# Kernel tuning notes

Hardware: AMD Instinct MI355X
Metric: run time of the kernel (lower is better)

Reference implementation:

```python
import jax, jax.numpy as jnp
import numpy as np

N = 100000
E = 1600000
F_IN = 128
F_OUT = 128
EPS = 1e-5


def setup_inputs() -> dict:
    key = jax.random.key(0)
    ks = jax.random.split(key, 6)
    x = jax.random.normal(ks[0], (N, F_IN), dtype=jnp.float32)
    edge_index = jax.random.randint(ks[1], (2, E), 0, N, dtype=jnp.int32)
    edge_weight = jax.random.uniform(ks[2], (E,), dtype=jnp.float32)
    gamma = jnp.ones((F_IN,), dtype=jnp.float32)
    beta = jnp.zeros((F_IN,), dtype=jnp.float32)
    W = jax.random.normal(ks[3], (F_OUT, F_IN), dtype=jnp.float32) * (1.0 / np.sqrt(F_IN))
    b = jnp.zeros((F_OUT,), dtype=jnp.float32)
    return {"x": x, "edge_index": edge_index, "edge_weight": edge_weight,
            "gamma": gamma, "beta": beta, "W": W, "b": b}


def reference(x, edge_index, edge_weight, gamma, beta, W, b):
    # LayerNorm (elementwise affine) + ReLU; dropout_mask=None (eval path)
    mean = jnp.mean(x, axis=-1, keepdims=True)
    var = jnp.mean(jnp.square(x - mean), axis=-1, keepdims=True)
    xn = (x - mean) * jax.lax.rsqrt(var + EPS) * gamma + beta
    xn = jax.nn.relu(xn)

    # GCNConv: linear first (PyG order), then normalized aggregation
    h = xn @ W.T  # [N, F_out]

    n = x.shape[0]
    row, col = edge_index[0], edge_index[1]
    # add self-loops with fill value 1.0 (improved=False)
    loop = jnp.arange(n, dtype=row.dtype)
    row = jnp.concatenate([row, loop])
    col = jnp.concatenate([col, loop])
    ew = jnp.concatenate([edge_weight, jnp.ones((n,), dtype=edge_weight.dtype)])

    # symmetric degree normalization: deg over destination (col)
    deg = jax.ops.segment_sum(ew, col, num_segments=n)
    dinv = jnp.where(deg > 0, jax.lax.rsqrt(deg), 0.0)
    norm = dinv[row] * ew * dinv[col]  # [E+N]

    # gather source features, weight, scatter-add to destinations
    msg = h[row] * norm[:, None]  # [E+N, F_out]
    out = jax.ops.segment_sum(msg, col, num_segments=n)
    return out + b
```

## Files before the change

kernel.cpp:

```cpp
#include <hip/hip_runtime.h>

#define NN 100000
#define EE 1600000
#define FDIM 128
#define EPS 1e-5f

#define NB1 ((NN + 255) / 256)

typedef __attribute__((ext_vector_type(8))) short s16x8;
typedef __attribute__((ext_vector_type(4))) float f32x4;

__device__ __forceinline__ unsigned short f2bf(float f) {
    unsigned int u = __float_as_uint(f);
    unsigned int r = u + 0x7FFFu + ((u >> 16) & 1u);
    return (unsigned short)(r >> 16);
}
__device__ __forceinline__ float bf_lo(unsigned int u) { return __uint_as_float(u << 16); }
__device__ __forceinline__ float bf_hi(unsigned int u) { return __uint_as_float(u & 0xFFFF0000u); }

__global__ __launch_bounds__(256) void k_deg0(unsigned long long* __restrict__ pk) {
    int i = blockIdx.x * 256 + threadIdx.x;
    if (i < NN) pk[i] = 0ULL;
}

__global__ __launch_bounds__(256) void k_deg_acc(const int* __restrict__ col,
                                                 const float* __restrict__ ew,
                                                 unsigned long long* __restrict__ pk) {
    int e = blockIdx.x * 256 + threadIdx.x;
    if (e < EE) {
        unsigned q = (unsigned)(ew[e] * 1048576.0f + 0.5f);
        atomicAdd(&pk[col[e]], (1ULL << 32) | (unsigned long long)q);
    }
}

__global__ __launch_bounds__(256) void k_scan1(const unsigned long long* __restrict__ pk,
                                               int* __restrict__ rowptr,
                                               int* __restrict__ bsum) {
    __shared__ int tmp[256];
    int tid = threadIdx.x;
    int i = blockIdx.x * 256 + tid;
    int v = (i < NN) ? (int)(pk[i] >> 32) : 0;
    tmp[tid] = v;
    __syncthreads();
    #pragma unroll
    for (int d = 1; d < 256; d <<= 1) {
        int t = (tid >= d) ? tmp[tid - d] : 0;
        __syncthreads();
        tmp[tid] += t;
        __syncthreads();
    }
    if (i < NN) rowptr[i] = tmp[tid] - v;
    if (tid == 255) bsum[blockIdx.x] = tmp[255];
}

__global__ __launch_bounds__(512) void k_scan2(int* __restrict__ bsum,
                                               int* __restrict__ bsumoff) {
    __shared__ int tmp[512];
    int tid = threadIdx.x;
    int v = (tid < NB1) ? bsum[tid] : 0;
    tmp[tid] = v;
    __syncthreads();
    #pragma unroll
    for (int d = 1; d < 512; d <<= 1) {
        int t = (tid >= d) ? tmp[tid - d] : 0;
        __syncthreads();
        tmp[tid] += t;
        __syncthreads();
    }
    if (tid < NB1) bsumoff[tid] = tmp[tid] - v;
}

__global__ __launch_bounds__(256) void k_scan3(int* __restrict__ rowptr,
                                               const int* __restrict__ bsumoff,
                                               int* __restrict__ cursor,
                                               const unsigned long long* __restrict__ pk,
                                               float* __restrict__ dinv) {
    int i = blockIdx.x * 256 + threadIdx.x;
    if (i < NN) {
        int rp = rowptr[i] + bsumoff[blockIdx.x];
        rowptr[i] = rp;
        cursor[i] = rp;
        float deg = 1.0f + (float)(unsigned)(pk[i] & 0xFFFFFFFFu) * (1.0f / 1048576.0f);
        dinv[i] = rsqrtf(deg);
    }
}

__global__ __launch_bounds__(256) void k_fill(const int* __restrict__ rowi,
                                              const int* __restrict__ coli,
                                              const float* __restrict__ ew,
                                              int* __restrict__ cursor,
                                              int2* __restrict__ sv) {
    int e = blockIdx.x * 256 + threadIdx.x;
    if (e < EE) {
        int pos = atomicAdd(&cursor[coli[e]], 1);
        sv[pos] = make_int2(rowi[e], __float_as_int(ew[e]));
    }
}

__global__ __launch_bounds__(256) void k_ln_gemm(const float* __restrict__ x,
                                                 const float* __restrict__ gamma,
                                                 const float* __restrict__ beta,
                                                 const float* __restrict__ W,
                                                 unsigned short* __restrict__ h) {
    __shared__ unsigned short sW[4 * 128 * 32];
    __shared__ unsigned short sA[4 * 64 * 32];

    int t = threadIdx.x;
    int lane = t & 63;
    int wv = t >> 6;
    int row0 = blockIdx.x * 64;

    for (int p = t; p < 512; p += 256) {
        int n = p >> 2, tt = p & 3;
        const float* src = &W[n * 128 + tt * 32];
        unsigned int* dst = (unsigned int*)&sW[tt * 4096 + n * 32];
        #pragma unroll
        for (int q = 0; q < 8; ++q) {
            float4 v = *(const float4*)&src[q * 4];
            dst[q * 2 + 0] = (unsigned)f2bf(v.x) | ((unsigned)f2bf(v.y) << 16);
            dst[q * 2 + 1] = (unsigned)f2bf(v.z) | ((unsigned)f2bf(v.w) << 16);
        }
    }

    int lane2 = lane * 2;
    float g0 = gamma[lane2], g1 = gamma[lane2 + 1];
    float be0 = beta[lane2],  be1 = beta[lane2 + 1];
    for (int i = 0; i < 16; ++i) {
        int r = wv * 16 + i;
        int row = row0 + r;
        float2 v = make_float2(0.f, 0.f);
        if (row < NN) v = *(const float2*)&x[(size_t)row * FDIM + lane2];
        float s  = v.x + v.y;
        float sq = v.x * v.x + v.y * v.y;
        #pragma unroll
        for (int d = 1; d < 64; d <<= 1) {
            s  += __shfl_xor(s, d, 64);
            sq += __shfl_xor(sq, d, 64);
        }
        float mean = s * (1.0f / 128.0f);
        float var  = sq * (1.0f / 128.0f) - mean * mean;
        float rstd = rsqrtf(var + EPS);
        float xn0 = fmaxf((v.x - mean) * rstd * g0 + be0, 0.f);
        float xn1 = fmaxf((v.y - mean) * rstd * g1 + be1, 0.f);
        if (row >= NN) { xn0 = 0.f; xn1 = 0.f; }
        *(unsigned int*)&sA[(lane >> 4) * 2048 + r * 32 + (lane2 & 31)] =
            (unsigned)f2bf(xn0) | ((unsigned)f2bf(xn1) << 16);
    }
    __syncthreads();

    f32x4 acc[8];
    #pragma unroll
    for (int j = 0; j < 8; ++j) acc[j] = (f32x4){0.f, 0.f, 0.f, 0.f};
    int arow = wv * 16 + (lane & 15);
    int kg = (lane >> 4) * 8;
    #pragma unroll
    for (int tt = 0; tt < 4; ++tt) {
        s16x8 a = *(const s16x8*)&sA[tt * 2048 + arow * 32 + kg];
        #pragma unroll
        for (int j = 0; j < 8; ++j) {
            s16x8 b = *(const s16x8*)&sW[tt * 4096 + (j * 16 + (lane & 15)) * 32 + kg];
            acc[j] = __builtin_amdgcn_mfma_f32_16x16x32_bf16(a, b, acc[j], 0, 0, 0);
        }
    }

    int orow = row0 + wv * 16 + (lane >> 4) * 4;
    int ocol = lane & 15;
    #pragma unroll
    for (int j = 0; j < 8; ++j) {
        #pragma unroll
        for (int i = 0; i < 4; ++i) {
            int g = orow + i;
            if (g < NN) h[(size_t)g * FDIM + j * 16 + ocol] = f2bf(acc[j][i]);
        }
    }
}

__global__ __launch_bounds__(256) void k_gather(const unsigned short* __restrict__ h,
                                                const float* __restrict__ dinv,
                                                const int* __restrict__ rowptr,
                                                const unsigned long long* __restrict__ pk,
                                                const int2* __restrict__ sv,
                                                const float* __restrict__ b,
                                                float* __restrict__ out) {
    int wv = threadIdx.x >> 6;
    int lane = threadIdx.x & 63;
    int n = blockIdx.x * 4 + wv;
    if (n >= NN) return;

    int f0 = lane * 2;
    float dc = dinv[n];
    unsigned int hv = *(const unsigned int*)&h[(size_t)n * FDIM + f0];
    float accx = bf_lo(hv) * dc;
    float accy = bf_hi(hv) * dc;

    int start = rowptr[n];
    int end = start + (int)(pk[n] >> 32);

    for (int base = start; base < end; base += 64) {
        int idx = base + lane;
        bool val = idx < end;
        int2 s = sv[val ? idx : start];
        float wn = val ? dinv[s.x] * __int_as_float(s.y) : 0.f;
        int m = min(64, end - base);
        int j = 0;
        for (; j + 3 < m; j += 4) {
            int   r0 = __shfl(s.x, j, 64),  r1 = __shfl(s.x, j + 1, 64);
            int   r2 = __shfl(s.x, j + 2, 64), r3 = __shfl(s.x, j + 3, 64);
            float w0 = __shfl(wn, j, 64),   w1 = __shfl(wn, j + 1, 64);
            float w2 = __shfl(wn, j + 2, 64), w3 = __shfl(wn, j + 3, 64);
            unsigned int a0 = *(const unsigned int*)&h[(size_t)r0 * FDIM + f0];
            unsigned int a1 = *(const unsigned int*)&h[(size_t)r1 * FDIM + f0];
            unsigned int a2 = *(const unsigned int*)&h[(size_t)r2 * FDIM + f0];
            unsigned int a3 = *(const unsigned int*)&h[(size_t)r3 * FDIM + f0];
            accx = fmaf(bf_lo(a0), w0, accx); accy = fmaf(bf_hi(a0), w0, accy);
            accx = fmaf(bf_lo(a1), w1, accx); accy = fmaf(bf_hi(a1), w1, accy);
            accx = fmaf(bf_lo(a2), w2, accx); accy = fmaf(bf_hi(a2), w2, accy);
            accx = fmaf(bf_lo(a3), w3, accx); accy = fmaf(bf_hi(a3), w3, accy);
        }
        for (; j < m; ++j) {
            int   rj = __shfl(s.x, j, 64);
            float wj = __shfl(wn, j, 64);
            unsigned int aj = *(const unsigned int*)&h[(size_t)rj * FDIM + f0];
            accx = fmaf(bf_lo(aj), wj, accx); accy = fmaf(bf_hi(aj), wj, accy);
        }
    }
    float2 bv = *(const float2*)&b[f0];
    *(float2*)&out[(size_t)n * FDIM + f0] =
        make_float2(fmaf(accx, dc, bv.x), fmaf(accy, dc, bv.y));
}

extern "C" void kernel_launch(void* const* d_in, const int* in_sizes, int n_in,
                              void* d_out, int out_size, void* d_ws, size_t ws_size,
                              hipStream_t stream) {
    const float* x     = (const float*)d_in[0];
    const int*   ei    = (const int*)d_in[1];
    const float* ew    = (const float*)d_in[2];
    const float* gamma = (const float*)d_in[3];
    const float* beta  = (const float*)d_in[4];
    const float* W     = (const float*)d_in[5];
    const float* b     = (const float*)d_in[6];
    float* out = (float*)d_out;

    char* p = (char*)d_ws;
    size_t off = 0;
    unsigned short* h = (unsigned short*)(p + off); off += (size_t)NN * FDIM * sizeof(unsigned short);
    unsigned long long* pk = (unsigned long long*)(p + off); off += (size_t)NN * sizeof(unsigned long long);
    float* dinv   = (float*)(p + off); off += (size_t)NN * sizeof(float);
    int*   cursor = (int*)  (p + off); off += (size_t)NN * sizeof(int);
    int*   rowptr = (int*)  (p + off); off += (size_t)NN * sizeof(int) + 16;
    int*   bsum   = (int*)  (p + off); off += 512 * sizeof(int);
    int*   bsumof = (int*)  (p + off); off += 512 * sizeof(int);
    int2*  sv     = (int2*) (p + off); off += (size_t)EE * sizeof(int2);
    (void)off; (void)ws_size;

    hipLaunchKernelGGL(k_deg0, dim3(NB1), dim3(256), 0, stream, pk);
    hipLaunchKernelGGL(k_deg_acc, dim3((EE + 255) / 256), dim3(256), 0, stream,
                       ei + EE, ew, pk);
    hipLaunchKernelGGL(k_ln_gemm, dim3((NN + 63) / 64), dim3(256), 0, stream,
                       x, gamma, beta, W, h);
    hipLaunchKernelGGL(k_scan1, dim3(NB1), dim3(256), 0, stream, pk, rowptr, bsum);
    hipLaunchKernelGGL(k_scan2, dim3(1), dim3(512), 0, stream, bsum, bsumof);
    hipLaunchKernelGGL(k_scan3, dim3(NB1), dim3(256), 0, stream, rowptr, bsumof, cursor, pk, dinv);
    hipLaunchKernelGGL(k_fill, dim3((EE + 255) / 256), dim3(256), 0, stream,
                       ei, ei + EE, ew, cursor, sv);
    hipLaunchKernelGGL(k_gather, dim3((NN + 3) / 4), dim3(256), 0, stream,
                       h, dinv, rowptr, pk, sv, b, out);
}
```

Measured before the change: 419.4 us.

## Reuse degree-atomic return as CSR slot, drop fill atomics; unroll gather by 8

The degree-counting atomic now returns the old count, which is stored per edge as that edge's slot within its destination segment. The fill pass then computes positions as rowptr plus that slot instead of doing a second atomic on a cursor array, and the cursor array is removed. The gather loop gains an 8-wide batch that issues eight independent loads before accumulating, to raise memory-level parallelism. This costs an extra 1.6M-int write and read of the slot array, and the 64-bit atomic must now return its value.

```diff
diff --git a/kernel.cpp b/kernel.cpp
--- a/kernel.cpp
+++ b/kernel.cpp
@@ -25,11 +25,13 @@
 
 __global__ __launch_bounds__(256) void k_deg_acc(const int* __restrict__ col,
                                                  const float* __restrict__ ew,
-                                                 unsigned long long* __restrict__ pk) {
+                                                 unsigned long long* __restrict__ pk,
+                                                 int* __restrict__ epos) {
     int e = blockIdx.x * 256 + threadIdx.x;
     if (e < EE) {
         unsigned q = (unsigned)(ew[e] * 1048576.0f + 0.5f);
-        atomicAdd(&pk[col[e]], (1ULL << 32) | (unsigned long long)q);
+        unsigned long long old = atomicAdd(&pk[col[e]], (1ULL << 32) | (unsigned long long)q);
+        epos[e] = (int)(old >> 32);
     }
 }
 
@@ -72,14 +74,11 @@
 
 __global__ __launch_bounds__(256) void k_scan3(int* __restrict__ rowptr,
                                                const int* __restrict__ bsumoff,
-                                               int* __restrict__ cursor,
                                                const unsigned long long* __restrict__ pk,
                                                float* __restrict__ dinv) {
     int i = blockIdx.x * 256 + threadIdx.x;
     if (i < NN) {
-        int rp = rowptr[i] + bsumoff[blockIdx.x];
-        rowptr[i] = rp;
-        cursor[i] = rp;
+        rowptr[i] += bsumoff[blockIdx.x];
         float deg = 1.0f + (float)(unsigned)(pk[i] & 0xFFFFFFFFu) * (1.0f / 1048576.0f);
         dinv[i] = rsqrtf(deg);
     }
@@ -88,11 +87,12 @@
 __global__ __launch_bounds__(256) void k_fill(const int* __restrict__ rowi,
                                               const int* __restrict__ coli,
                                               const float* __restrict__ ew,
-                                              int* __restrict__ cursor,
+                                              const int* __restrict__ rowptr,
+                                              const int* __restrict__ epos,
                                               int2* __restrict__ sv) {
     int e = blockIdx.x * 256 + threadIdx.x;
     if (e < EE) {
-        int pos = atomicAdd(&cursor[coli[e]], 1);
+        int pos = rowptr[coli[e]] + epos[e];
         sv[pos] = make_int2(rowi[e], __float_as_int(ew[e]));
     }
 }
@@ -203,25 +203,44 @@
         float wn = val ? dinv[s.x] * __int_as_float(s.y) : 0.f;
         int m = min(64, end - base);
         int j = 0;
+        for (; j + 7 < m; j += 8) {
+            int ar[8]; float aw[8]; unsigned int av[8];
+            #pragma unroll
+            for (int q = 0; q < 8; ++q) {
+                ar[q] = __shfl(s.x, j + q, 64);
+                aw[q] = __shfl(wn, j + q, 64);
+            }
+            #pragma unroll
+            for (int q = 0; q < 8; ++q)
+                av[q] = *(const unsigned int*)&h[(size_t)ar[q] * FDIM + f0];
+            #pragma unroll
+            for (int q = 0; q < 8; ++q) {
+                accx = fmaf(bf_lo(av[q]), aw[q], accx);
+                accy = fmaf(bf_hi(av[q]), aw[q], accy);
+            }
+        }
         for (; j + 3 < m; j += 4) {
-            int   r0 = __shfl(s.x, j, 64),  r1 = __shfl(s.x, j + 1, 64);
-            int   r2 = __shfl(s.x, j + 2, 64), r3 = __shfl(s.x, j + 3, 64);
-            float w0 = __shfl(wn, j, 64),   w1 = __shfl(wn, j + 1, 64);
-            float w2 = __shfl(wn, j + 2, 64), w3 = __shfl(wn, j + 3, 64);
-            unsigned int a0 = *(const unsigned int*)&h[(size_t)r0 * FDIM + f0];
-            unsigned int a1 = *(const unsigned int*)&h[(size_t)r1 * FDIM + f0];
-            unsigned int a2 = *(const unsigned int*)&h[(size_t)r2 * FDIM + f0];
-            unsigned int a3 = *(const unsigned int*)&h[(size_t)r3 * FDIM + f0];
-            accx = fmaf(bf_lo(a0), w0, accx); accy = fmaf(bf_hi(a0), w0, accy);
-            accx = fmaf(bf_lo(a1), w1, accx); accy = fmaf(bf_hi(a1), w1, accy);
-            accx = fmaf(bf_lo(a2), w2, accx); accy = fmaf(bf_hi(a2), w2, accy);
-            accx = fmaf(bf_lo(a3), w3, accx); accy = fmaf(bf_hi(a3), w3, accy);
+            int ar[4]; float aw[4]; unsigned int av[4];
+            #pragma unroll
+            for (int q = 0; q < 4; ++q) {
+                ar[q] = __shfl(s.x, j + q, 64);
+                aw[q] = __shfl(wn, j + q, 64);
+            }
+            #pragma unroll
+            for (int q = 0; q < 4; ++q)
+                av[q] = *(const unsigned int*)&h[(size_t)ar[q] * FDIM + f0];
+            #pragma unroll
+            for (int q = 0; q < 4; ++q) {
+                accx = fmaf(bf_lo(av[q]), aw[q], accx);
+                accy = fmaf(bf_hi(av[q]), aw[q], accy);
+            }
         }
         for (; j < m; ++j) {
             int   rj = __shfl(s.x, j, 64);
             float wj = __shfl(wn, j, 64);
             unsigned int aj = *(const unsigned int*)&h[(size_t)rj * FDIM + f0];
-            accx = fmaf(bf_lo(aj), wj, accx); accy = fmaf(bf_hi(aj), wj, accy);
+            accx = fmaf(bf_lo(aj), wj, accx);
+            accy = fmaf(bf_hi(aj), wj, accy);
         }
     }
     float2 bv = *(const float2*)&b[f0];
@@ -246,23 +265,23 @@
     unsigned short* h = (unsigned short*)(p + off); off += (size_t)NN * FDIM * sizeof(unsigned short);
     unsigned long long* pk = (unsigned long long*)(p + off); off += (size_t)NN * sizeof(unsigned long long);
     float* dinv   = (float*)(p + off); off += (size_t)NN * sizeof(float);
-    int*   cursor = (int*)  (p + off); off += (size_t)NN * sizeof(int);
     int*   rowptr = (int*)  (p + off); off += (size_t)NN * sizeof(int) + 16;
     int*   bsum   = (int*)  (p + off); off += 512 * sizeof(int);
     int*   bsumof = (int*)  (p + off); off += 512 * sizeof(int);
+    int*   epos   = (int*)  (p + off); off += (size_t)EE * sizeof(int);
     int2*  sv     = (int2*) (p + off); off += (size_t)EE * sizeof(int2);
     (void)off; (void)ws_size;
 
     hipLaunchKernelGGL(k_deg0, dim3(NB1), dim3(256), 0, stream, pk);
     hipLaunchKernelGGL(k_deg_acc, dim3((EE + 255) / 256), dim3(256), 0, stream,
-                       ei + EE, ew, pk);
+                       ei + EE, ew, pk, epos);
     hipLaunchKernelGGL(k_ln_gemm, dim3((NN + 63) / 64), dim3(256), 0, stream,
                        x, gamma, beta, W, h);
     hipLaunchKernelGGL(k_scan1, dim3(NB1), dim3(256), 0, stream, pk, rowptr, bsum);
     hipLaunchKernelGGL(k_scan2, dim3(1), dim3(512), 0, stream, bsum, bsumof);
-    hipLaunchKernelGGL(k_scan3, dim3(NB1), dim3(256), 0, stream, rowptr, bsumof, cursor, pk, dinv);
+    hipLaunchKernelGGL(k_scan3, dim3(NB1), dim3(256), 0, stream, rowptr, bsumof, pk, dinv);
     hipLaunchKernelGGL(k_fill, dim3((EE + 255) / 256), dim3(256), 0, stream,
-                       ei, ei + EE, ew, cursor, sv);
+                       ei, ei + EE, ew, rowptr, epos, sv);
     hipLaunchKernelGGL(k_gather, dim3((NN + 3) / 4), dim3(256), 0, stream,
                        h, dinv, rowptr, pk, sv, b, out);
 }
```

Result: faster. 351.0 us (-16.3%).
